# Optimization experiments

Measured on AMD Instinct MI355X. Metric: run time of the kernel, lower is better.

## Reference

```python
import jax, jax.numpy as jnp
import numpy as np

G_NUMS = 30      # group_nums
G_SIZE = 100     # group_size (also neighborhood_size)
BETA = 1.0
EPS = 1e-9


def setup_inputs() -> dict:
    key = jax.random.key(0)
    pointclouds = jax.random.normal(key, (8, 131072, 3), dtype=jnp.float32)
    return {"pointclouds": pointclouds}


def _knn_gather(points, queries, k):
    """points [b,N,3], queries [b,G,3] -> k nearest points per query [b,G,k,3]."""
    # squared distances [b,G,N]
    d2 = (
        jnp.sum(queries * queries, axis=-1)[..., None]
        - 2.0 * jnp.einsum("bgd,bnd->bgn", queries, points)
        + jnp.sum(points * points, axis=-1)[:, None, :]
    )
    _, idx = jax.lax.top_k(-d2, k)                    # [b,G,k]
    nbrs = jax.vmap(lambda p, i: p[i])(points, idx)   # [b,G,k,3]
    return nbrs


def reference(pointclouds):
    b, N, _ = pointclouds.shape
    # --- group_points: uniform-stride sampled centers, k-NN groups, group means ---
    stride = N // G_NUMS
    centers = pointclouds[:, ::stride][:, :G_NUMS]                 # [b,G,3]
    grouped = _knn_gather(pointclouds, centers, G_SIZE)            # [b,G,K,3]
    group_means = jnp.mean(grouped, axis=2)                        # [b,G,3]

    # --- estimate_pointcloud_local_coord_frames: per-group 3x3 PCA ---
    nbrs = _knn_gather(pointclouds, group_means, G_SIZE)           # [b,G,K,3]
    mu = jnp.mean(nbrs, axis=2, keepdims=True)
    X = nbrs - mu
    cov = jnp.einsum("bgkd,bgke->bgde", X, X) / G_SIZE             # [b,G,3,3]
    curvatures, frames = jnp.linalg.eigh(cov)                      # eigvals ascending

    # --- elongated-shape loss ---
    denom = curvatures[..., 0] + curvatures[..., 1] + curvatures[..., 2] + EPS
    first_vec = curvatures[..., 2] / denom
    second_vec = curvatures[..., 1] / denom
    elongated_shape_loss = -jnp.sum(first_vec - second_vec) / b

    # --- angular smoothness cost over group means / principal directions ---
    dirs = frames[..., :, 2]                                       # [b,G,3] largest-eig direction
    dm = jnp.sum(
        (group_means[:, :, None, :] - group_means[:, None, :, :]) ** 2, axis=-1
    )                                                              # [b,G,G]
    dm = dm + jnp.eye(G_NUMS, dtype=dm.dtype) * jnp.float32(1e30)  # exclude self
    j = jnp.argmin(dm, axis=-1)                                    # [b,G]
    dirs_j = jnp.take_along_axis(dirs, j[..., None], axis=1)       # [b,G,3]
    cos = jnp.sum(dirs * dirs_j, axis=-1)
    dlo_smooth_loss = jnp.mean(1.0 - cos * cos)                    # sign-invariant angle cost

    return elongated_shape_loss + BETA * dlo_smooth_loss
```

## Files before the change

kernel.cpp:

```cpp
#include <hip/hip_runtime.h>
#include <math.h>

#define N_PTS     131072
#define G_NUMS    30
#define G_SIZE    100
#define PT_STRIDE (N_PTS / G_NUMS)
#define TPB       512
#define NWAVES    (TPB / 64)
#define BINS      4096
#define SHIFT     20
#define SAMPLE_GRPS 1024
#define RANK_CUT  32
#define CAP       3072
#define TIE_CAP   64

__device__ __forceinline__ float dist2f(float px, float py, float pz,
                                        float qx, float qy, float qz) {
    float dx = px - qx, dy = py - qy, dz = pz - qz;
    return fmaf(dx, dx, fmaf(dy, dy, dz * dz));
}

__device__ __forceinline__ unsigned find_bin(unsigned* s_hist, unsigned* s_wsum,
                                             unsigned* s_T, unsigned rank,
                                             int tid, int lane, int wid) {
    unsigned hv[8], csum = 0;
#pragma unroll
    for (int j = 0; j < 8; j++) { hv[j] = s_hist[tid * 8 + j]; csum += hv[j]; }
    unsigned inc = csum;
#pragma unroll
    for (int off = 1; off < 64; off <<= 1) {
        unsigned n = __shfl_up(inc, off);
        if (lane >= off) inc += n;
    }
    __syncthreads();
    if (lane == 63) s_wsum[wid] = inc;
    __syncthreads();
    unsigned base = 0;
    for (int w = 0; w < wid; w++) base += s_wsum[w];
    unsigned c = base + inc - csum;
#pragma unroll
    for (int j = 0; j < 8; j++) {
        if (c < rank && c + hv[j] >= rank) *s_T = (unsigned)(tid * 8 + j);
        c += hv[j];
    }
    __syncthreads();
    return *s_T;
}

__global__ __launch_bounds__(TPB)
void fused_knn_kernel(const float* __restrict__ pts,
                      float* __restrict__ out_mean, float* __restrict__ out_cov,
                      int B) {
    __shared__ unsigned s_hist[BINS];
    __shared__ unsigned s_wsum[NWAVES];
    __shared__ unsigned s_T;
    __shared__ int s_ns, s_nd, s_nt;
    __shared__ unsigned s_u[CAP];
    __shared__ int s_idx[CAP];
    __shared__ int s_sel[G_SIZE];
    __shared__ unsigned s_tu[TIE_CAP];
    __shared__ int s_ti[TIE_CAP];
    __shared__ float s_acc[3], s_cov[6], s_q[3];

    const int blk = blockIdx.x;
    const int b = blk % B;
    const int g = blk / B;
    const int gi = b * G_NUMS + g;
    const float* __restrict__ P = pts + (size_t)b * (N_PTS * 3);
    const float4* __restrict__ P4 = (const float4*)P;
    const int tid = threadIdx.x;
    const int lane = tid & 63, wid = tid >> 6;

    if (tid == 0) {
        const float* q = P + (size_t)g * PT_STRIDE * 3;
        s_q[0] = q[0]; s_q[1] = q[1]; s_q[2] = q[2];
    }

    for (int phase = 0; phase < 2; ++phase) {
        __syncthreads();
        const float qx = s_q[0], qy = s_q[1], qz = s_q[2];

        for (int j = tid; j < BINS; j += TPB) s_hist[j] = 0u;
        if (tid == 0) { s_ns = 0; s_nd = 0; s_nt = 0; s_T = 0u; }
        if (tid < 3) s_acc[tid] = 0.f;
        if (tid < 6) s_cov[tid] = 0.f;
        __syncthreads();

        for (int grp = tid; grp < SAMPLE_GRPS; grp += TPB) {
            float4 f0 = P4[3 * grp + 0];
            float4 f1 = P4[3 * grp + 1];
            float4 f2 = P4[3 * grp + 2];
            unsigned u0 = __float_as_uint(dist2f(f0.x, f0.y, f0.z, qx, qy, qz));
            unsigned u1 = __float_as_uint(dist2f(f0.w, f1.x, f1.y, qx, qy, qz));
            unsigned u2 = __float_as_uint(dist2f(f1.z, f1.w, f2.x, qx, qy, qz));
            unsigned u3 = __float_as_uint(dist2f(f2.y, f2.z, f2.w, qx, qy, qz));
            atomicAdd(&s_hist[u0 >> SHIFT], 1u);
            atomicAdd(&s_hist[u1 >> SHIFT], 1u);
            atomicAdd(&s_hist[u2 >> SHIFT], 1u);
            atomicAdd(&s_hist[u3 >> SHIFT], 1u);
        }
        __syncthreads();
        unsigned Tc = find_bin(s_hist, s_wsum, &s_T, RANK_CUT, tid, lane, wid);
        const unsigned tau = (Tc >= BINS - 1) ? 0xFFFFFFFFu : ((Tc + 1) << SHIFT);
        for (int j = tid; j < BINS; j += TPB) s_hist[j] = 0u;
        __syncthreads();

#pragma unroll 4
        for (int grp = tid; grp < N_PTS / 4; grp += TPB) {
            float4 f0 = P4[3 * grp + 0];
            float4 f1 = P4[3 * grp + 1];
            float4 f2 = P4[3 * grp + 2];
            unsigned u0 = __float_as_uint(dist2f(f0.x, f0.y, f0.z, qx, qy, qz));
            unsigned u1 = __float_as_uint(dist2f(f0.w, f1.x, f1.y, qx, qy, qz));
            unsigned u2 = __float_as_uint(dist2f(f1.z, f1.w, f2.x, qx, qy, qz));
            unsigned u3 = __float_as_uint(dist2f(f2.y, f2.z, f2.w, qx, qy, qz));
            int i0 = grp * 4;
            if (u0 < tau) { int p = atomicAdd(&s_ns, 1); if (p < CAP) { s_u[p] = u0; s_idx[p] = i0; } }
            if (u1 < tau) { int p = atomicAdd(&s_ns, 1); if (p < CAP) { s_u[p] = u1; s_idx[p] = i0 + 1; } }
            if (u2 < tau) { int p = atomicAdd(&s_ns, 1); if (p < CAP) { s_u[p] = u2; s_idx[p] = i0 + 2; } }
            if (u3 < tau) { int p = atomicAdd(&s_ns, 1); if (p < CAP) { s_u[p] = u3; s_idx[p] = i0 + 3; } }
        }
        __syncthreads();
        int S = s_ns; if (S > CAP) S = CAP;

        unsigned hb = 32u - (unsigned)__clz(tau - 1u);
        unsigned s2 = hb > 12u ? hb - 12u : 0u;
        for (int i = tid; i < S; i += TPB) atomicAdd(&s_hist[s_u[i] >> s2], 1u);
        __syncthreads();
        unsigned T2 = find_bin(s_hist, s_wsum, &s_T, G_SIZE, tid, lane, wid);
        const unsigned lo = T2 << s2;

        for (int i = tid; i < S; i += TPB) {
            unsigned u = s_u[i];
            if (u < lo) {
                int p = atomicAdd(&s_nd, 1);
                if (p < G_SIZE) s_sel[p] = s_idx[i];
            } else if ((u >> s2) == T2) {
                int p = atomicAdd(&s_nt, 1);
                if (p < TIE_CAP) { s_tu[p] = u; s_ti[p] = s_idx[i]; }
            }
        }
        __syncthreads();
        if (tid == 0) {
            int nd = s_nd; if (nd > G_SIZE) nd = G_SIZE;
            int need = G_SIZE - nd;
            int ec = s_nt; if (ec > TIE_CAP) ec = TIE_CAP;
            for (int a = 0; a < need && a < ec; ++a) {
                int best = a;
                for (int j = a + 1; j < ec; ++j)
                    if (s_tu[j] < s_tu[best] ||
                        (s_tu[j] == s_tu[best] && s_ti[j] < s_ti[best])) best = j;
                unsigned tu = s_tu[best]; s_tu[best] = s_tu[a]; s_tu[a] = tu;
                int ti = s_ti[best]; s_ti[best] = s_ti[a]; s_ti[a] = ti;
                s_sel[nd + a] = s_ti[a];
            }
        }
        __syncthreads();

        float px = 0.f, py = 0.f, pz = 0.f;
        if (tid < G_SIZE) {
            const float* pp = P + 3 * (size_t)s_sel[tid];
            px = pp[0]; py = pp[1]; pz = pp[2];
            atomicAdd(&s_acc[0], px);
            atomicAdd(&s_acc[1], py);
            atomicAdd(&s_acc[2], pz);
        }
        __syncthreads();

        if (phase == 0) {
            if (tid < 3) {
                float m = s_acc[tid] * (1.0f / G_SIZE);
                out_mean[(size_t)gi * 3 + tid] = m;
                s_q[tid] = m;
            }
        } else {
            float mx = s_acc[0] * (1.0f / G_SIZE);
            float my = s_acc[1] * (1.0f / G_SIZE);
            float mz = s_acc[2] * (1.0f / G_SIZE);
            if (tid < G_SIZE) {
                float x = px - mx, y = py - my, z = pz - mz;
                atomicAdd(&s_cov[0], x * x);
                atomicAdd(&s_cov[1], x * y);
                atomicAdd(&s_cov[2], x * z);
                atomicAdd(&s_cov[3], y * y);
                atomicAdd(&s_cov[4], y * z);
                atomicAdd(&s_cov[5], z * z);
            }
            __syncthreads();
            if (tid < 6) out_cov[(size_t)gi * 6 + tid] = s_cov[tid] * (1.0f / G_SIZE);
        }
    }
}

__device__ void eig3(const float cf[6], double lam_out[3], double dir_out[3]) {
    double a[3][3], v[3][3];
    a[0][0] = cf[0]; a[0][1] = cf[1]; a[0][2] = cf[2];
    a[1][0] = cf[1]; a[1][1] = cf[3]; a[1][2] = cf[4];
    a[2][0] = cf[2]; a[2][1] = cf[4]; a[2][2] = cf[5];
    for (int i = 0; i < 3; i++)
        for (int j = 0; j < 3; j++) v[i][j] = (i == j) ? 1.0 : 0.0;

    for (int sweep = 0; sweep < 12; sweep++) {
        double off = a[0][1] * a[0][1] + a[0][2] * a[0][2] + a[1][2] * a[1][2];
        if (off == 0.0) break;
        for (int p = 0; p < 2; p++) {
            for (int q = p + 1; q < 3; q++) {
                double apq = a[p][q];
                if (apq == 0.0) continue;
                double app = a[p][p], aqq = a[q][q];
                double theta = (aqq - app) / (2.0 * apq);
                double t = (theta >= 0.0 ? 1.0 : -1.0) /
                           (fabs(theta) + sqrt(theta * theta + 1.0));
                double c = 1.0 / sqrt(t * t + 1.0);
                double s = t * c;
                a[p][p] = app - t * apq;
                a[q][q] = aqq + t * apq;
                a[p][q] = 0.0; a[q][p] = 0.0;
                for (int r = 0; r < 3; r++) {
                    if (r == p || r == q) continue;
                    double arp = a[r][p], arq = a[r][q];
                    a[r][p] = c * arp - s * arq; a[p][r] = a[r][p];
                    a[r][q] = s * arp + c * arq; a[q][r] = a[r][q];
                }
                for (int r = 0; r < 3; r++) {
                    double vrp = v[r][p], vrq = v[r][q];
                    v[r][p] = c * vrp - s * vrq;
                    v[r][q] = s * vrp + c * vrq;
                }
            }
        }
    }
    double l0 = a[0][0], l1 = a[1][1], l2 = a[2][2];
    int i0 = 0, i1 = 1, i2 = 2;
    if (l0 > l1) { double t = l0; l0 = l1; l1 = t; int ti = i0; i0 = i1; i1 = ti; }
    if (l1 > l2) { double t = l1; l1 = l2; l2 = t; int ti = i1; i1 = i2; i2 = ti; }
    if (l0 > l1) { double t = l0; l0 = l1; l1 = t; int ti = i0; i0 = i1; i1 = ti; }
    lam_out[0] = l0; lam_out[1] = l1; lam_out[2] = l2;
    dir_out[0] = v[0][i2]; dir_out[1] = v[1][i2]; dir_out[2] = v[2][i2];
}

__global__ __launch_bounds__(256)
void finalize_kernel(const float* __restrict__ gmeans, const float* __restrict__ covs,
                     float* __restrict__ out, int B) {
    const int tid = threadIdx.x;
    const int NG = B * G_NUMS;
    __shared__ float s_dir[256][3];
    __shared__ float s_gm[256][3];
    __shared__ float s_pe[4];
    __shared__ float s_ps[4];

    float et = 0.f;
    if (tid < NG) {
        float cf[6];
#pragma unroll
        for (int j = 0; j < 6; j++) cf[j] = covs[tid * 6 + j];
        double lam[3], dir[3];
        eig3(cf, lam, dir);
        double denom = lam[0] + lam[1] + lam[2] + 1e-9;
        et = (float)((lam[2] - lam[1]) / denom);
        s_dir[tid][0] = (float)dir[0];
        s_dir[tid][1] = (float)dir[1];
        s_dir[tid][2] = (float)dir[2];
        s_gm[tid][0] = gmeans[tid * 3 + 0];
        s_gm[tid][1] = gmeans[tid * 3 + 1];
        s_gm[tid][2] = gmeans[tid * 3 + 2];
    }
    __syncthreads();

    float st = 0.f;
    if (tid < NG) {
        int b = tid / G_NUMS, g = tid % G_NUMS;
        float gx = s_gm[tid][0], gy = s_gm[tid][1], gz = s_gm[tid][2];
        float bd = 3.4e38f; int bj = 0;
        for (int gg = 0; gg < G_NUMS; gg++) {
            if (gg == g) continue;
            int o = b * G_NUMS + gg;
            float dx = gx - s_gm[o][0];
            float dy = gy - s_gm[o][1];
            float dz = gz - s_gm[o][2];
            float d = dx * dx + dy * dy + dz * dz;
            if (d < bd) { bd = d; bj = gg; }
        }
        int o = b * G_NUMS + bj;
        float cosv = s_dir[tid][0] * s_dir[o][0] +
                     s_dir[tid][1] * s_dir[o][1] +
                     s_dir[tid][2] * s_dir[o][2];
        st = 1.f - cosv * cosv;
    }

    float e = et, s2 = st;
#pragma unroll
    for (int off = 32; off > 0; off >>= 1) {
        e += __shfl_down(e, off);
        s2 += __shfl_down(s2, off);
    }
    int lane = tid & 63, wid = tid >> 6;
    if (lane == 0) { s_pe[wid] = e; s_ps[wid] = s2; }
    __syncthreads();
    if (tid == 0) {
        float se = 0.f, ss = 0.f;
        for (int w = 0; w < 4; w++) { se += s_pe[w]; ss += s_ps[w]; }
        out[0] = -se / (float)B + ss / (float)NG;
    }
}

extern "C" void kernel_launch(void* const* d_in, const int* in_sizes, int n_in,
                              void* d_out, int out_size, void* d_ws, size_t ws_size,
                              hipStream_t stream) {
    const float* pts = (const float*)d_in[0];
    float* out = (float*)d_out;
    float* ws = (float*)d_ws;
    int B = in_sizes[0] / (N_PTS * 3);
    float* gmeans = ws;
    float* covs = ws + (size_t)B * G_NUMS * 3;

    dim3 grid(B * G_NUMS);
    fused_knn_kernel<<<grid, TPB, 0, stream>>>(pts, gmeans, covs, B);
    finalize_kernel<<<1, 256, 0, stream>>>(gmeans, covs, out, B);
}
```

Baseline: 162.2 us.

## Split fused kNN into multi-kernel pipeline sharing point chunks across all groups

Replaces the one-block-per-group kernel, which streams the whole point cloud once per query in each phase, with a pipeline of kernels. A tau kernel computes per-group thresholds, and a filter kernel loads each point chunk once and tests it against all 30 queries of its batch. Survivors are written to global memory through per-block shared buffers, and select kernels then finish the top-k, means and covariance. This cuts redundant global reads and raises parallelism, at the cost of extra launches, global atomics, a survivor buffer in workspace, and a smaller rank cut and capacity that could drop candidates.

Measured after the change: 183.6 us. 13.2% more time.

```diff
diff --git a/kernel.cpp b/kernel.cpp
--- a/kernel.cpp
+++ b/kernel.cpp
@@ -5,14 +5,14 @@
 #define G_NUMS    30
 #define G_SIZE    100
 #define PT_STRIDE (N_PTS / G_NUMS)
-#define TPB       512
-#define NWAVES    (TPB / 64)
 #define BINS      4096
 #define SHIFT     20
 #define SAMPLE_GRPS 1024
-#define RANK_CUT  32
-#define CAP       3072
+#define RANK_CUT  24
+#define CAP       2048
+#define CAPB      64
 #define TIE_CAP   64
+#define CHUNK_PTS 2048
 
 __device__ __forceinline__ float dist2f(float px, float py, float pz,
                                         float qx, float qy, float qz) {
@@ -47,148 +47,220 @@
     return *s_T;
 }
 
-__global__ __launch_bounds__(TPB)
-void fused_knn_kernel(const float* __restrict__ pts,
-                      float* __restrict__ out_mean, float* __restrict__ out_cov,
-                      int B) {
+__global__ __launch_bounds__(512)
+void tau0_kernel(const float* __restrict__ pts, float4* __restrict__ qtau0,
+                 int* __restrict__ counts, int B) {
     __shared__ unsigned s_hist[BINS];
-    __shared__ unsigned s_wsum[NWAVES];
+    __shared__ unsigned s_wsum[8];
     __shared__ unsigned s_T;
-    __shared__ int s_ns, s_nd, s_nt;
-    __shared__ unsigned s_u[CAP];
-    __shared__ int s_idx[CAP];
+    const int blk = blockIdx.x;
+    const int b = blk % B, g = blk / B;
+    const int gi = b * G_NUMS + g;
+    const float* __restrict__ P = pts + (size_t)b * (N_PTS * 3);
+    const float4* __restrict__ P4 = (const float4*)P;
+    const int tid = threadIdx.x, lane = tid & 63, wid = tid >> 6;
+    const float qx = P[(size_t)g * PT_STRIDE * 3 + 0];
+    const float qy = P[(size_t)g * PT_STRIDE * 3 + 1];
+    const float qz = P[(size_t)g * PT_STRIDE * 3 + 2];
+
+    for (int j = tid; j < BINS; j += 512) s_hist[j] = 0u;
+    if (tid == 0) s_T = 0u;
+    __syncthreads();
+    for (int grp = tid; grp < SAMPLE_GRPS; grp += 512) {
+        float4 f0 = P4[3 * grp + 0];
+        float4 f1 = P4[3 * grp + 1];
+        float4 f2 = P4[3 * grp + 2];
+        atomicAdd(&s_hist[__float_as_uint(dist2f(f0.x, f0.y, f0.z, qx, qy, qz)) >> SHIFT], 1u);
+        atomicAdd(&s_hist[__float_as_uint(dist2f(f0.w, f1.x, f1.y, qx, qy, qz)) >> SHIFT], 1u);
+        atomicAdd(&s_hist[__float_as_uint(dist2f(f1.z, f1.w, f2.x, qx, qy, qz)) >> SHIFT], 1u);
+        atomicAdd(&s_hist[__float_as_uint(dist2f(f2.y, f2.z, f2.w, qx, qy, qz)) >> SHIFT], 1u);
+    }
+    __syncthreads();
+    unsigned Tc = find_bin(s_hist, s_wsum, &s_T, RANK_CUT, tid, lane, wid);
+    unsigned tau = (Tc >= BINS - 1) ? 0xFFFFFFFFu : ((Tc + 1) << SHIFT);
+    if (tid == 0) {
+        qtau0[gi] = make_float4(qx, qy, qz, __uint_as_float(tau));
+        counts[gi] = 0;
+    }
+}
+
+__global__ __launch_bounds__(512)
+void filter_kernel(const float* __restrict__ pts, const float4* __restrict__ qtau,
+                   int* __restrict__ counts, uint2* __restrict__ surv, int B) {
+    __shared__ float4 s_qt[G_NUMS];
+    __shared__ int s_cnt[G_NUMS];
+    __shared__ uint2 s_buf[G_NUMS][CAPB];
+
+    const int blk = blockIdx.x;
+    const int b = blk % B;
+    const int chunk = blk / B;
+    const float4* __restrict__ P4 = (const float4*)(pts + (size_t)b * (N_PTS * 3));
+    const int tid = threadIdx.x;
+    const int lane = tid & 63, wid = tid >> 6;
+
+    if (tid < G_NUMS) { s_qt[tid] = qtau[b * G_NUMS + tid]; s_cnt[tid] = 0; }
+    __syncthreads();
+
+    const int i0 = chunk * CHUNK_PTS + tid * 4;
+    float4 f0 = P4[chunk * (CHUNK_PTS * 3 / 4) + tid * 3 + 0];
+    float4 f1 = P4[chunk * (CHUNK_PTS * 3 / 4) + tid * 3 + 1];
+    float4 f2 = P4[chunk * (CHUNK_PTS * 3 / 4) + tid * 3 + 2];
+    const float x0 = f0.x, y0 = f0.y, z0 = f0.z;
+    const float x1 = f0.w, y1 = f1.x, z1 = f1.y;
+    const float x2 = f1.z, y2 = f1.w, z2 = f2.x;
+    const float x3 = f2.y, y3 = f2.z, z3 = f2.w;
+
+    for (int g = 0; g < G_NUMS; ++g) {
+        float4 qt = s_qt[g];
+        const unsigned tau = __float_as_uint(qt.w);
+        unsigned u0 = __float_as_uint(dist2f(x0, y0, z0, qt.x, qt.y, qt.z));
+        unsigned u1 = __float_as_uint(dist2f(x1, y1, z1, qt.x, qt.y, qt.z));
+        unsigned u2 = __float_as_uint(dist2f(x2, y2, z2, qt.x, qt.y, qt.z));
+        unsigned u3 = __float_as_uint(dist2f(x3, y3, z3, qt.x, qt.y, qt.z));
+#pragma unroll
+        for (int j = 0; j < 4; ++j) {
+            unsigned u = j == 0 ? u0 : j == 1 ? u1 : j == 2 ? u2 : u3;
+            if (u < tau) {
+                int p = atomicAdd(&s_cnt[g], 1);
+                if (p < CAPB) {
+                    s_buf[g][p] = make_uint2(u, (unsigned)(i0 + j));
+                } else {
+                    int gp = atomicAdd(&counts[b * G_NUMS + g], 1);
+                    if (gp < CAP)
+                        surv[(size_t)(b * G_NUMS + g) * CAP + gp] =
+                            make_uint2(u, (unsigned)(i0 + j));
+                }
+            }
+        }
+    }
+    __syncthreads();
+
+    for (int g = wid; g < G_NUMS; g += 8) {
+        int n = s_cnt[g]; if (n > CAPB) n = CAPB;
+        int base = 0;
+        if (lane == 0 && n > 0) base = atomicAdd(&counts[b * G_NUMS + g], n);
+        base = __shfl(base, 0);
+        for (int i = lane; i < n; i += 64) {
+            int p = base + i;
+            if (p < CAP) surv[(size_t)(b * G_NUMS + g) * CAP + p] = s_buf[g][i];
+        }
+    }
+}
+
+template <int PHASE>
+__global__ __launch_bounds__(512)
+void select_kernel(const float* __restrict__ pts,
+                   const float4* __restrict__ qtau_cur,
+                   float4* __restrict__ qtau_next,
+                   const uint2* __restrict__ surv, int* __restrict__ counts,
+                   float* __restrict__ gmeans, float* __restrict__ covs, int B) {
+    __shared__ unsigned s_hist[BINS];
+    __shared__ unsigned s_wsum[8];
+    __shared__ unsigned s_T;
+    __shared__ int s_nd, s_nt;
     __shared__ int s_sel[G_SIZE];
     __shared__ unsigned s_tu[TIE_CAP];
     __shared__ int s_ti[TIE_CAP];
-    __shared__ float s_acc[3], s_cov[6], s_q[3];
+    __shared__ float s_acc[3], s_cov[6];
 
     const int blk = blockIdx.x;
-    const int b = blk % B;
-    const int g = blk / B;
+    const int b = blk % B, g = blk / B;
     const int gi = b * G_NUMS + g;
     const float* __restrict__ P = pts + (size_t)b * (N_PTS * 3);
     const float4* __restrict__ P4 = (const float4*)P;
-    const int tid = threadIdx.x;
-    const int lane = tid & 63, wid = tid >> 6;
-
+    const int tid = threadIdx.x, lane = tid & 63, wid = tid >> 6;
+
+    const float4 qt = qtau_cur[gi];
+    const unsigned tau = __float_as_uint(qt.w);
+    int S = counts[gi]; if (S > CAP) S = CAP;
+    const uint2* __restrict__ sv = surv + (size_t)gi * CAP;
+
+    for (int j = tid; j < BINS; j += 512) s_hist[j] = 0u;
+    if (tid == 0) { s_T = 0u; s_nd = 0; s_nt = 0; }
+    if (tid < 3) s_acc[tid] = 0.f;
+    if (tid < 6) s_cov[tid] = 0.f;
+    __syncthreads();
+
+    unsigned hb = 32u - (unsigned)__clz(tau - 1u);
+    unsigned sh = hb > 12u ? hb - 12u : 0u;
+    for (int i = tid; i < S; i += 512) atomicAdd(&s_hist[sv[i].x >> sh], 1u);
+    __syncthreads();
+    unsigned T2 = find_bin(s_hist, s_wsum, &s_T, G_SIZE, tid, lane, wid);
+    const unsigned lo = T2 << sh;
+
+    for (int i = tid; i < S; i += 512) {
+        unsigned u = sv[i].x;
+        if (u < lo) {
+            int p = atomicAdd(&s_nd, 1);
+            if (p < G_SIZE) s_sel[p] = (int)sv[i].y;
+        } else if ((u >> sh) == T2) {
+            int p = atomicAdd(&s_nt, 1);
+            if (p < TIE_CAP) { s_tu[p] = u; s_ti[p] = (int)sv[i].y; }
+        }
+    }
+    __syncthreads();
     if (tid == 0) {
-        const float* q = P + (size_t)g * PT_STRIDE * 3;
-        s_q[0] = q[0]; s_q[1] = q[1]; s_q[2] = q[2];
-    }
-
-    for (int phase = 0; phase < 2; ++phase) {
+        int nd = s_nd; if (nd > G_SIZE) nd = G_SIZE;
+        int need = G_SIZE - nd;
+        int ec = s_nt; if (ec > TIE_CAP) ec = TIE_CAP;
+        for (int a = 0; a < need && a < ec; ++a) {
+            int best = a;
+            for (int j = a + 1; j < ec; ++j)
+                if (s_tu[j] < s_tu[best] ||
+                    (s_tu[j] == s_tu[best] && s_ti[j] < s_ti[best])) best = j;
+            unsigned tu = s_tu[best]; s_tu[best] = s_tu[a]; s_tu[a] = tu;
+            int ti = s_ti[best]; s_ti[best] = s_ti[a]; s_ti[a] = ti;
+            s_sel[nd + a] = s_ti[a];
+        }
+    }
+    __syncthreads();
+
+    float px = 0.f, py = 0.f, pz = 0.f;
+    if (tid < G_SIZE) {
+        const float* pp = P + 3 * (size_t)s_sel[tid];
+        px = pp[0]; py = pp[1]; pz = pp[2];
+        atomicAdd(&s_acc[0], px);
+        atomicAdd(&s_acc[1], py);
+        atomicAdd(&s_acc[2], pz);
+    }
+    __syncthreads();
+    const float mx = s_acc[0] * (1.0f / G_SIZE);
+    const float my = s_acc[1] * (1.0f / G_SIZE);
+    const float mz = s_acc[2] * (1.0f / G_SIZE);
+
+    if (PHASE == 0) {
+        if (tid < 3) gmeans[gi * 3 + tid] = (tid == 0 ? mx : tid == 1 ? my : mz);
+        for (int j = tid; j < BINS; j += 512) s_hist[j] = 0u;
+        if (tid == 0) s_T = 0u;
         __syncthreads();
-        const float qx = s_q[0], qy = s_q[1], qz = s_q[2];
-
-        for (int j = tid; j < BINS; j += TPB) s_hist[j] = 0u;
-        if (tid == 0) { s_ns = 0; s_nd = 0; s_nt = 0; s_T = 0u; }
-        if (tid < 3) s_acc[tid] = 0.f;
-        if (tid < 6) s_cov[tid] = 0.f;
-        __syncthreads();
-
-        for (int grp = tid; grp < SAMPLE_GRPS; grp += TPB) {
+        for (int grp = tid; grp < SAMPLE_GRPS; grp += 512) {
             float4 f0 = P4[3 * grp + 0];
             float4 f1 = P4[3 * grp + 1];
             float4 f2 = P4[3 * grp + 2];
-            unsigned u0 = __float_as_uint(dist2f(f0.x, f0.y, f0.z, qx, qy, qz));
-            unsigned u1 = __float_as_uint(dist2f(f0.w, f1.x, f1.y, qx, qy, qz));
-            unsigned u2 = __float_as_uint(dist2f(f1.z, f1.w, f2.x, qx, qy, qz));
-            unsigned u3 = __float_as_uint(dist2f(f2.y, f2.z, f2.w, qx, qy, qz));
-            atomicAdd(&s_hist[u0 >> SHIFT], 1u);
-            atomicAdd(&s_hist[u1 >> SHIFT], 1u);
-            atomicAdd(&s_hist[u2 >> SHIFT], 1u);
-            atomicAdd(&s_hist[u3 >> SHIFT], 1u);
+            atomicAdd(&s_hist[__float_as_uint(dist2f(f0.x, f0.y, f0.z, mx, my, mz)) >> SHIFT], 1u);
+            atomicAdd(&s_hist[__float_as_uint(dist2f(f0.w, f1.x, f1.y, mx, my, mz)) >> SHIFT], 1u);
+            atomicAdd(&s_hist[__float_as_uint(dist2f(f1.z, f1.w, f2.x, mx, my, mz)) >> SHIFT], 1u);
+            atomicAdd(&s_hist[__float_as_uint(dist2f(f2.y, f2.z, f2.w, mx, my, mz)) >> SHIFT], 1u);
         }
         __syncthreads();
         unsigned Tc = find_bin(s_hist, s_wsum, &s_T, RANK_CUT, tid, lane, wid);
-        const unsigned tau = (Tc >= BINS - 1) ? 0xFFFFFFFFu : ((Tc + 1) << SHIFT);
-        for (int j = tid; j < BINS; j += TPB) s_hist[j] = 0u;
+        unsigned tau1 = (Tc >= BINS - 1) ? 0xFFFFFFFFu : ((Tc + 1) << SHIFT);
+        if (tid == 0) {
+            qtau_next[gi] = make_float4(mx, my, mz, __uint_as_float(tau1));
+            counts[gi] = 0;
+        }
+    } else {
+        if (tid < G_SIZE) {
+            float x = px - mx, y = py - my, z = pz - mz;
+            atomicAdd(&s_cov[0], x * x);
+            atomicAdd(&s_cov[1], x * y);
+            atomicAdd(&s_cov[2], x * z);
+            atomicAdd(&s_cov[3], y * y);
+            atomicAdd(&s_cov[4], y * z);
+            atomicAdd(&s_cov[5], z * z);
+        }
         __syncthreads();
-
-#pragma unroll 4
-        for (int grp = tid; grp < N_PTS / 4; grp += TPB) {
-            float4 f0 = P4[3 * grp + 0];
-            float4 f1 = P4[3 * grp + 1];
-            float4 f2 = P4[3 * grp + 2];
-            unsigned u0 = __float_as_uint(dist2f(f0.x, f0.y, f0.z, qx, qy, qz));
-            unsigned u1 = __float_as_uint(dist2f(f0.w, f1.x, f1.y, qx, qy, qz));
-            unsigned u2 = __float_as_uint(dist2f(f1.z, f1.w, f2.x, qx, qy, qz));
-            unsigned u3 = __float_as_uint(dist2f(f2.y, f2.z, f2.w, qx, qy, qz));
-            int i0 = grp * 4;
-            if (u0 < tau) { int p = atomicAdd(&s_ns, 1); if (p < CAP) { s_u[p] = u0; s_idx[p] = i0; } }
-            if (u1 < tau) { int p = atomicAdd(&s_ns, 1); if (p < CAP) { s_u[p] = u1; s_idx[p] = i0 + 1; } }
-            if (u2 < tau) { int p = atomicAdd(&s_ns, 1); if (p < CAP) { s_u[p] = u2; s_idx[p] = i0 + 2; } }
-            if (u3 < tau) { int p = atomicAdd(&s_ns, 1); if (p < CAP) { s_u[p] = u3; s_idx[p] = i0 + 3; } }
-        }
-        __syncthreads();
-        int S = s_ns; if (S > CAP) S = CAP;
-
-        unsigned hb = 32u - (unsigned)__clz(tau - 1u);
-        unsigned s2 = hb > 12u ? hb - 12u : 0u;
-        for (int i = tid; i < S; i += TPB) atomicAdd(&s_hist[s_u[i] >> s2], 1u);
-        __syncthreads();
-        unsigned T2 = find_bin(s_hist, s_wsum, &s_T, G_SIZE, tid, lane, wid);
-        const unsigned lo = T2 << s2;
-
-        for (int i = tid; i < S; i += TPB) {
-            unsigned u = s_u[i];
-            if (u < lo) {
-                int p = atomicAdd(&s_nd, 1);
-                if (p < G_SIZE) s_sel[p] = s_idx[i];
-            } else if ((u >> s2) == T2) {
-                int p = atomicAdd(&s_nt, 1);
-                if (p < TIE_CAP) { s_tu[p] = u; s_ti[p] = s_idx[i]; }
-            }
-        }
-        __syncthreads();
-        if (tid == 0) {
-            int nd = s_nd; if (nd > G_SIZE) nd = G_SIZE;
-            int need = G_SIZE - nd;
-            int ec = s_nt; if (ec > TIE_CAP) ec = TIE_CAP;
-            for (int a = 0; a < need && a < ec; ++a) {
-                int best = a;
-                for (int j = a + 1; j < ec; ++j)
-                    if (s_tu[j] < s_tu[best] ||
-                        (s_tu[j] == s_tu[best] && s_ti[j] < s_ti[best])) best = j;
-                unsigned tu = s_tu[best]; s_tu[best] = s_tu[a]; s_tu[a] = tu;
-                int ti = s_ti[best]; s_ti[best] = s_ti[a]; s_ti[a] = ti;
-                s_sel[nd + a] = s_ti[a];
-            }
-        }
-        __syncthreads();
-
-        float px = 0.f, py = 0.f, pz = 0.f;
-        if (tid < G_SIZE) {
-            const float* pp = P + 3 * (size_t)s_sel[tid];
-            px = pp[0]; py = pp[1]; pz = pp[2];
-            atomicAdd(&s_acc[0], px);
-            atomicAdd(&s_acc[1], py);
-            atomicAdd(&s_acc[2], pz);
-        }
-        __syncthreads();
-
-        if (phase == 0) {
-            if (tid < 3) {
-                float m = s_acc[tid] * (1.0f / G_SIZE);
-                out_mean[(size_t)gi * 3 + tid] = m;
-                s_q[tid] = m;
-            }
-        } else {
-            float mx = s_acc[0] * (1.0f / G_SIZE);
-            float my = s_acc[1] * (1.0f / G_SIZE);
-            float mz = s_acc[2] * (1.0f / G_SIZE);
-            if (tid < G_SIZE) {
-                float x = px - mx, y = py - my, z = pz - mz;
-                atomicAdd(&s_cov[0], x * x);
-                atomicAdd(&s_cov[1], x * y);
-                atomicAdd(&s_cov[2], x * z);
-                atomicAdd(&s_cov[3], y * y);
-                atomicAdd(&s_cov[4], y * z);
-                atomicAdd(&s_cov[5], z * z);
-            }
-            __syncthreads();
-            if (tid < 6) out_cov[(size_t)gi * 6 + tid] = s_cov[tid] * (1.0f / G_SIZE);
-        }
+        if (tid < 6) covs[gi * 6 + tid] = s_cov[tid] * (1.0f / G_SIZE);
     }
 }
 
@@ -309,12 +381,20 @@
                               hipStream_t stream) {
     const float* pts = (const float*)d_in[0];
     float* out = (float*)d_out;
-    float* ws = (float*)d_ws;
     int B = in_sizes[0] / (N_PTS * 3);
-    float* gmeans = ws;
-    float* covs = ws + (size_t)B * G_NUMS * 3;
-
-    dim3 grid(B * G_NUMS);
-    fused_knn_kernel<<<grid, TPB, 0, stream>>>(pts, gmeans, covs, B);
+    const int NG = B * G_NUMS;
+
+    float4* qtau0 = (float4*)d_ws;
+    float4* qtau1 = qtau0 + NG;
+    float* gmeans = (float*)(qtau1 + NG);
+    float* covs = gmeans + NG * 3;
+    int* counts = (int*)(covs + NG * 6);
+    uint2* surv = (uint2*)(counts + 256);
+
+    tau0_kernel<<<NG, 512, 0, stream>>>(pts, qtau0, counts, B);
+    filter_kernel<<<B * (N_PTS / CHUNK_PTS), 512, 0, stream>>>(pts, qtau0, counts, surv, B);
+    select_kernel<0><<<NG, 512, 0, stream>>>(pts, qtau0, qtau1, surv, counts, gmeans, covs, B);
+    filter_kernel<<<B * (N_PTS / CHUNK_PTS), 512, 0, stream>>>(pts, qtau1, counts, surv, B);
+    select_kernel<1><<<NG, 512, 0, stream>>>(pts, qtau1, nullptr, surv, counts, gmeans, covs, B);
     finalize_kernel<<<1, 256, 0, stream>>>(gmeans, covs, out, B);
 }
```
